# Kernel optimization log

Measured on AMD Instinct MI355X. Metric: run time of the kernel, lower is better.

Reference implementation:

```python
import jax, jax.numpy as jnp
import numpy as np

CUTOFF_RADIUS = 5.0
ETA = 0.5
ZETA = 1.0
LAMBDA = 1.0


def setup_inputs() -> dict:
    key = jax.random.key(0)
    k1, k2 = jax.random.split(key)
    B, N = 16, 96
    distance_vectors = jax.random.normal(k1, (B, N, N, 3), dtype=jnp.float32)
    # positive distances in (0, 1): within cutoff, no exact zeros off-diagonal
    distances = jax.random.uniform(k2, (B, N, N), dtype=jnp.float32)
    return {"distance_vectors": distance_vectors, "distances": distances}


def reference(distance_vectors, distances):
    # cosines[b,i,j,k] = <r_ij, r_jk> / (d_ij * d_jk)
    dot_products = jnp.einsum('bijd,bjkd->bijk', distance_vectors, distance_vectors)
    magnitudes = jnp.einsum('bij,bjk->bijk', distances, distances)
    cosines = dot_products / magnitudes

    cosine_term = (1.0 + LAMBDA * cosines) ** ZETA
    cosine_term = jnp.nan_to_num(cosine_term, nan=0.0, posinf=0.0, neginf=0.0)

    # exponent[b,i,j,k] = d_ij^2 + d_ik^2 + d_jk^2
    d2 = distances ** 2
    exponent = d2[..., :, :, None] + d2[..., :, None, :] + d2[..., None, :, :]
    exponential_term = jnp.exp(-ETA * exponent)

    # smooth cutoff radial function
    radials = jnp.tanh(1.0 - distances / CUTOFF_RADIUS) ** 3
    radials = jnp.where(distances <= CUTOFF_RADIUS, radials, jnp.zeros_like(distances))
    radial_term = (radials[..., :, :, None]
                   * radials[..., :, None, :]
                   * radials[..., None, :, :])

    coefficient = 2.0 ** (1.0 - ZETA)
    return coefficient * (cosine_term * exponential_term * radial_term).sum(axis=(-1, -2))
```

## Files before the change

### kernel.cpp

```cpp
#include <hip/hip_runtime.h>
#include <hip/hip_bf16.h>


#define B 16
#define N 96
#define KP 128
#define TI 4
#define JS 8
#define JC (N / JS)
#define P2_THREADS 128

__global__ void g4_prep(const float* __restrict__ dv,
                        const float* __restrict__ dist,
                        float4* __restrict__ W,
                        float* __restrict__ out) {
    int idx = blockIdx.x * blockDim.x + threadIdx.x;
    if (idx < B * N) out[idx] = 0.f;
    if (idx >= B * N * KP) return;
    int k   = idx & (KP - 1);
    int row = idx >> 7;
    float4 w = make_float4(0.f, 0.f, 0.f, 0.f);
    if (k < N) {
        int src = row * N + k;
        float d = dist[src];
        float e2 = expf(-2.0f * (1.0f - d * 0.2f));
        float r  = (1.0f - e2) / (1.0f + e2);
        float f  = expf(-0.5f * d * d) * r * r * r;
        float q  = f / d;
        w.x = f;
        w.y = dv[src * 3 + 0] * q;
        w.z = dv[src * 3 + 1] * q;
        w.w = dv[src * 3 + 2] * q;
    }
    W[idx] = w;
}

__global__ __launch_bounds__(P2_THREADS)
void g4_contract(const float4* __restrict__ W, float* __restrict__ out) {
    const int bi   = blockIdx.x;
    const int js   = bi % JS;
    const int rest = bi / JS;
    const int b    = rest / (N / TI);
    const int i0   = (rest % (N / TI)) * TI;
    const int j0   = js * JC;
    const int t    = threadIdx.x;

    __shared__ float4 rowI[TI][JC];

    const float4* Wb = W + (size_t)b * N * KP;

    for (int e = t; e < TI * JC; e += P2_THREADS) {
        int ii = e / JC, jj = e % JC;
        rowI[ii][jj] = Wb[(i0 + ii) * KP + j0 + jj];
    }

    float fik[TI];
#pragma unroll
    for (int ii = 0; ii < TI; ++ii)
        fik[ii] = Wb[(i0 + ii) * KP + t].x;

    __syncthreads();

    float acc[TI] = {0.f, 0.f, 0.f, 0.f};
#pragma unroll
    for (int jj = 0; jj < JC; ++jj) {
        float4 wj = Wb[(j0 + jj) * KP + t];
#pragma unroll
        for (int ii = 0; ii < TI; ++ii) {
            float4 ri = rowI[ii][jj];
            float inner = ri.x * wj.x + ri.y * wj.y + ri.z * wj.z + ri.w * wj.w;
            acc[ii] = fmaf(fik[ii], inner, acc[ii]);
        }
    }

    __shared__ float red[TI][2];
#pragma unroll
    for (int ii = 0; ii < TI; ++ii) {
        float v = acc[ii];
#pragma unroll
        for (int off = 32; off > 0; off >>= 1)
            v += __shfl_down(v, off);
        if ((t & 63) == 0) red[ii][t >> 6] = v;
    }
    __syncthreads();
    if (t < TI)
        atomicAdd(&out[b * N + i0 + t], red[t][0] + red[t][1]);
}

extern "C" void kernel_launch(void* const* d_in, const int* in_sizes, int n_in,
                              void* d_out, int out_size, void* d_ws, size_t ws_size,
                              hipStream_t stream) {
    const float* dv   = (const float*)d_in[0];
    const float* dist = (const float*)d_in[1];
    float*  out = (float*)d_out;
    float4* W   = (float4*)d_ws;

    {
        int total = B * N * KP;
        int thr = 256;
        int blk = (total + thr - 1) / thr;
        g4_prep<<<blk, thr, 0, stream>>>(dv, dist, W, out);
    }
    {
        int blk = B * (N / TI) * JS;
        g4_contract<<<blk, P2_THREADS, 0, stream>>>(W, out);
    }
}
```

Before: 69.84 us.

## Fuse weight precompute into contraction kernel, recomputing per-block

Removes the separate prep kernel and the float4 workspace. Each contraction block now computes its own radial/exp weights and scaled vectors straight from the inputs, and the output is zeroed with a memset. This drops one kernel launch and the round trip through the workspace. In exchange, every block recomputes the exp/tanh weights for its j rows, which is redundant work across the 24 i-tiles, and reads dv with uncoalesced stride-3 loads.

```diff
diff --git a/kernel.cpp b/kernel.cpp
--- a/kernel.cpp
+++ b/kernel.cpp
@@ -4,39 +4,21 @@
 
 #define B 16
 #define N 96
-#define KP 128
 #define TI 4
 #define JS 8
 #define JC (N / JS)
 #define P2_THREADS 128
 
-__global__ void g4_prep(const float* __restrict__ dv,
-                        const float* __restrict__ dist,
-                        float4* __restrict__ W,
-                        float* __restrict__ out) {
-    int idx = blockIdx.x * blockDim.x + threadIdx.x;
-    if (idx < B * N) out[idx] = 0.f;
-    if (idx >= B * N * KP) return;
-    int k   = idx & (KP - 1);
-    int row = idx >> 7;
-    float4 w = make_float4(0.f, 0.f, 0.f, 0.f);
-    if (k < N) {
-        int src = row * N + k;
-        float d = dist[src];
-        float e2 = expf(-2.0f * (1.0f - d * 0.2f));
-        float r  = (1.0f - e2) / (1.0f + e2);
-        float f  = expf(-0.5f * d * d) * r * r * r;
-        float q  = f / d;
-        w.x = f;
-        w.y = dv[src * 3 + 0] * q;
-        w.z = dv[src * 3 + 1] * q;
-        w.w = dv[src * 3 + 2] * q;
-    }
-    W[idx] = w;
+__device__ __forceinline__ float g4_f(float d) {
+    float e2 = expf(-2.0f * (1.0f - d * 0.2f));
+    float r  = (1.0f - e2) / (1.0f + e2);
+    return expf(-0.5f * d * d) * r * r * r;
 }
 
 __global__ __launch_bounds__(P2_THREADS)
-void g4_contract(const float4* __restrict__ W, float* __restrict__ out) {
+void g4_fused(const float* __restrict__ dv,
+              const float* __restrict__ dist,
+              float* __restrict__ out) {
     const int bi   = blockIdx.x;
     const int js   = bi % JS;
     const int rest = bi / JS;
@@ -47,28 +29,52 @@
 
     __shared__ float4 rowI[TI][JC];
 
-    const float4* Wb = W + (size_t)b * N * KP;
-
-    for (int e = t; e < TI * JC; e += P2_THREADS) {
-        int ii = e / JC, jj = e % JC;
-        rowI[ii][jj] = Wb[(i0 + ii) * KP + j0 + jj];
+    if (t < TI * JC) {
+        int ii = t / JC, jj = t % JC;
+        int src = (b * N + i0 + ii) * N + (j0 + jj);
+        float d = dist[src];
+        float f = g4_f(d);
+        float q = f / d;
+        rowI[ii][jj] = make_float4(f, dv[src * 3 + 0] * q,
+                                      dv[src * 3 + 1] * q,
+                                      dv[src * 3 + 2] * q);
     }
 
-    float fik[TI];
+    float4 wj[JC];
+    float  fik[TI];
+    if (t < N) {
 #pragma unroll
-    for (int ii = 0; ii < TI; ++ii)
-        fik[ii] = Wb[(i0 + ii) * KP + t].x;
+        for (int jj = 0; jj < JC; ++jj) {
+            int src = (b * N + j0 + jj) * N + t;
+            float d = dist[src];
+            float f = g4_f(d);
+            float q = f / d;
+            wj[jj] = make_float4(f, dv[src * 3 + 0] * q,
+                                    dv[src * 3 + 1] * q,
+                                    dv[src * 3 + 2] * q);
+        }
+#pragma unroll
+        for (int ii = 0; ii < TI; ++ii)
+            fik[ii] = g4_f(dist[(b * N + i0 + ii) * N + t]);
+    } else {
+#pragma unroll
+        for (int jj = 0; jj < JC; ++jj)
+            wj[jj] = make_float4(0.f, 0.f, 0.f, 0.f);
+#pragma unroll
+        for (int ii = 0; ii < TI; ++ii)
+            fik[ii] = 0.f;
+    }
 
     __syncthreads();
 
     float acc[TI] = {0.f, 0.f, 0.f, 0.f};
 #pragma unroll
     for (int jj = 0; jj < JC; ++jj) {
-        float4 wj = Wb[(j0 + jj) * KP + t];
 #pragma unroll
         for (int ii = 0; ii < TI; ++ii) {
             float4 ri = rowI[ii][jj];
-            float inner = ri.x * wj.x + ri.y * wj.y + ri.z * wj.z + ri.w * wj.w;
+            float inner = ri.x * wj[jj].x + ri.y * wj[jj].y
+                        + ri.z * wj[jj].z + ri.w * wj[jj].w;
             acc[ii] = fmaf(fik[ii], inner, acc[ii]);
         }
     }
@@ -92,17 +98,10 @@
                               hipStream_t stream) {
     const float* dv   = (const float*)d_in[0];
     const float* dist = (const float*)d_in[1];
-    float*  out = (float*)d_out;
-    float4* W   = (float4*)d_ws;
+    float* out = (float*)d_out;
 
-    {
-        int total = B * N * KP;
-        int thr = 256;
-        int blk = (total + thr - 1) / thr;
-        g4_prep<<<blk, thr, 0, stream>>>(dv, dist, W, out);
-    }
-    {
-        int blk = B * (N / TI) * JS;
-        g4_contract<<<blk, P2_THREADS, 0, stream>>>(W, out);
-    }
+    hipMemsetAsync(out, 0, (size_t)out_size * sizeof(float), stream);
+
+    int blk = B * (N / TI) * JS;
+    g4_fused<<<blk, P2_THREADS, 0, stream>>>(dv, dist, out);
 }
```

After: 77.41 us. +10.8%, slower.
